# Performance work log

Hardware: AMD Instinct MI355X
Metric: run time of the kernel (lower is better)

## Reference

```python
import jax, jax.numpy as jnp
import numpy as np

WS = 8          # window_size
SHIFT = WS // 2 # shift for 'SW' type
HEADS = 6
HD = 32


def setup_inputs() -> dict:
    key = jax.random.key(0)
    ks = jax.random.split(key, 6)
    return {
        "x": jax.random.normal(ks[0], (4, 256, 256, 192), jnp.float32),
        "w_qkv": jax.random.normal(ks[1], (192, 576), jnp.float32) * 0.02,
        "b_qkv": jax.random.normal(ks[2], (576,), jnp.float32) * 0.02,
        "rel_pos": jax.random.normal(ks[3], (HEADS, 2 * WS - 1, 2 * WS - 1), jnp.float32) * 0.02,
        "w_out": jax.random.normal(ks[4], (192, 192), jnp.float32) * 0.02,
        "b_out": jax.random.normal(ks[5], (192,), jnp.float32) * 0.02,
    }


def reference(x, w_qkv, b_qkv, rel_pos, w_out, b_out):
    b, h, w, c = x.shape
    scale = HD ** (-0.5)
    wa = WS * WS  # window area
    # shifted-window roll
    x = jnp.roll(x, (-SHIFT, -SHIFT), axis=(1, 2))
    hw, ww = h // WS, w // WS
    nw = hw * ww
    # partition into windows: [b, nw, wa, c]
    xw = x.reshape(b, hw, WS, ww, WS, c).transpose(0, 1, 3, 2, 4, 5).reshape(b, nw, wa, c)
    qkv = xw @ w_qkv + b_qkv                       # [b, nw, wa, 3c]
    qkv = qkv.reshape(b, nw, wa, 3, HEADS, HD)
    q = qkv[..., 0, :, :] * scale
    k = qkv[..., 1, :, :]
    v = qkv[..., 2, :, :]
    attn = jnp.einsum('bnqhd,bnkhd->bnhqk', q, k)  # [b, nw, heads, wa, wa]
    # relative position bias
    coords = jnp.stack(jnp.meshgrid(jnp.arange(WS), jnp.arange(WS), indexing='ij')).reshape(2, -1).T  # [wa,2]
    rel = coords[:, None, :] - coords[None, :, :] + WS - 1   # [wa, wa, 2]
    bias = rel_pos[:, rel[..., 0], rel[..., 1]]              # [heads, wa, wa]
    attn = attn + bias[None, None]
    # shift mask (only last window masked, per the module's generate_mask)
    s = WS - SHIFT
    mask = jnp.zeros((nw, wa, wa), bool)
    mask = mask.at[-1, :s, s:].set(True).at[-1, s:, :s].set(True)
    attn = jnp.where(mask[None, :, None], -jnp.inf, attn)
    attn = jax.nn.softmax(attn, axis=-1)
    out = jnp.einsum('bnhqk,bnkhd->bnqhd', attn, v)          # [b, nw, wa, heads, hd]
    out = out.reshape(b, hw, ww, WS, WS, c).transpose(0, 1, 3, 2, 4, 5).reshape(b, h, w, c)
    out = out @ w_out + b_out
    out = jnp.roll(out, (SHIFT, SHIFT), axis=(1, 2))
    return out
```

## Files before the change

### kernel.cpp

```cpp
#include <hip/hip_runtime.h>
#include <hip/hip_bf16.h>

typedef __attribute__((ext_vector_type(8))) short short8;
typedef __attribute__((ext_vector_type(4))) float f32x4;

#define MFMA(a, b, c) __builtin_amdgcn_mfma_f32_16x16x32_bf16((a), (b), (c), 0, 0, 0)

namespace {
constexpr int IMG = 256;
constexpr int NWIN = 1024;
constexpr float SCALE = 0.17677669529663687f;
constexpr float L2E   = 1.4426950408889634f;
}

__device__ __forceinline__ unsigned pack2(float a, float b) {
    __hip_bfloat162 h = __float22bfloat162_rn(make_float2(a, b));
    union { __hip_bfloat162 h; unsigned u; } v; v.h = h;
    return v.u;
}

__global__ __launch_bounds__(256)
void prep_all(const float* __restrict__ w_qkv, const float* __restrict__ w_out,
              const float* __restrict__ rel_pos, const float* __restrict__ b_qkv,
              unsigned short* __restrict__ wqT, unsigned short* __restrict__ woT,
              float* __restrict__ biasf, float* __restrict__ bq2) {
    const int bx = blockIdx.x;
    const int t  = threadIdx.x;
    if (bx < 72) {
        __shared__ float tile[32][65];
        const float* in; unsigned short* out; int N, scale_n; float scale; int tx, ty;
        if (bx < 54) { in = w_qkv; out = wqT; N = 576; scale_n = 192; scale = SCALE; tx = bx % 9; ty = bx / 9; }
        else { const int b2 = bx - 54; in = w_out; out = woT; N = 192; scale_n = 0; scale = 1.0f; tx = b2 % 3; ty = b2 / 3; }
        const int nb = tx * 64, kb = ty * 32;
        const int tn = t & 63, tk = t >> 6;
#pragma unroll
        for (int p = 0; p < 8; ++p)
            tile[p * 4 + tk][tn] = in[(size_t)(kb + p * 4 + tk) * N + nb + tn];
        __syncthreads();
        const int n = t >> 2, kc = (t & 3) * 8;
        const float s = (nb + n) < scale_n ? scale : 1.0f;
        uint4 u;
        u.x = pack2(tile[kc + 0][n] * s, tile[kc + 1][n] * s);
        u.y = pack2(tile[kc + 2][n] * s, tile[kc + 3][n] * s);
        u.z = pack2(tile[kc + 4][n] * s, tile[kc + 5][n] * s);
        u.w = pack2(tile[kc + 6][n] * s, tile[kc + 7][n] * s);
        *(uint4*)(out + (size_t)(nb + n) * 192 + kb + kc) = u;
    } else {
        const int o = (bx - 72) * 256 + t;
        const int k = o & 63, q = (o >> 6) & 63, h = o >> 12;
        const int qy = q >> 3, qx = q & 7, ky = k >> 3, kx = k & 7;
        const float bv = rel_pos[h * 225 + (qy - ky + 7) * 15 + (qx - kx + 7)] * L2E;
        biasf[o] = bv;
        const bool masked = (q < 4) != (k < 4);
        biasf[24576 + o] = masked ? -30000.0f : bv;
        if (bx == 72) {
            for (int i = t; i < 576; i += 256)
                bq2[i] = b_qkv[i] * (i < 192 ? SCALE : 1.0f);
        }
    }
}

__global__ __launch_bounds__(256, 3)
void wmsa_fused(const float* __restrict__ x,
                const float* __restrict__ bq2,
                const float* __restrict__ biasf,
                const unsigned short* __restrict__ wqT,
                const unsigned short* __restrict__ woT,
                const float* __restrict__ b_out,
                float* __restrict__ out) {
    __shared__ unsigned short x_s[64][200];
    __shared__ unsigned short qp_s[64][72];
    __shared__ unsigned short kp_s[64][72];
    __shared__ unsigned short vT_s[64][72];

    const int tid = threadIdx.x;
    const int w   = tid >> 6;
    const int l   = tid & 63;
    const int l15 = l & 15, lg = l >> 4;
    const int wing = blockIdx.x;
    const int b   = wing >> 10;
    const int win = wing & (NWIN - 1);
    const int wy  = win >> 5, wx = win & 31;
    const float* bias_t = biasf + ((win == NWIN - 1) ? 24576 : 0);

    {
        const int t  = tid >> 2;
        const int c0 = tid & 3;
        const int pr = ((wy << 3) + (t >> 3) + 4) & (IMG - 1);
        const int pc = ((wx << 3) + (t & 7) + 4) & (IMG - 1);
        const float* xrow = x + ((size_t)((b * IMG + pr) * IMG + pc)) * 192;
#pragma unroll
        for (int i = 0; i < 12; ++i) {
            const int c = c0 + 4 * i;
            const float4 xv = *reinterpret_cast<const float4*>(xrow + c * 4);
            uint2 pk; pk.x = pack2(xv.x, xv.y); pk.y = pack2(xv.z, xv.w);
            *(uint2*)(&x_s[t][c * 4]) = pk;
        }
    }
    __syncthreads();

    const int h_loc = w >> 1;
    const int qt0   = 2 * (w & 1);

    f32x4 g2[3][4];
#pragma unroll
    for (int mi = 0; mi < 3; ++mi) {
        const float4 bo = *reinterpret_cast<const float4*>(b_out + 16 * (w + 4 * mi) + 4 * lg);
        const f32x4 c0 = {bo.x, bo.y, bo.z, bo.w};
#pragma unroll
        for (int nt = 0; nt < 4; ++nt) g2[mi][nt] = c0;
    }

#pragma unroll 1
    for (int g = 0; g < 3; ++g) {
        f32x4 aq[3][4];
        const unsigned short* wp[3];
#pragma unroll
        for (int ci = 0; ci < 3; ++ci) {
            const int t = w + 4 * ci;
            const int which = t >> 2, sub = t & 3;
            const int hh = sub >> 1, d0 = (sub & 1) * 16;
            const int grow = which * 192 + (2 * g + hh) * 32 + d0 + l15;
            wp[ci] = wqT + (size_t)grow * 192 + lg * 8;
            f32x4 c0;
            if (which < 2) {
                const float4 b4 = *reinterpret_cast<const float4*>(
                    bq2 + which * 192 + (2 * g + hh) * 32 + d0 + 4 * lg);
                c0 = f32x4{b4.x, b4.y, b4.z, b4.w};
            } else {
                const float bb = bq2[384 + (2 * g + hh) * 32 + d0 + l15];
                c0 = f32x4{bb, bb, bb, bb};
            }
#pragma unroll
            for (int nt = 0; nt < 4; ++nt) aq[ci][nt] = c0;
        }

        __builtin_amdgcn_s_setprio(1);
#pragma unroll
        for (int ks = 0; ks < 6; ++ks) {
            short8 xf[4];
#pragma unroll
            for (int nt = 0; nt < 4; ++nt)
                xf[nt] = *(const short8*)(&x_s[16 * nt + l15][ks * 32 + lg * 8]);
#pragma unroll
            for (int ci = 0; ci < 3; ++ci) {
                const short8 wf = *(const short8*)wp[ci];
                wp[ci] += 32;
                if (ci < 2 ? ((w + 4 * ci) >> 2) < 2 : ((w + 8) >> 2) < 2) {
#pragma unroll
                    for (int nt = 0; nt < 4; ++nt) aq[ci][nt] = MFMA(wf, xf[nt], aq[ci][nt]);
                } else {
#pragma unroll
                    for (int nt = 0; nt < 4; ++nt) aq[ci][nt] = MFMA(xf[nt], wf, aq[ci][nt]);
                }
            }
        }
        __builtin_amdgcn_s_setprio(0);

#pragma unroll
        for (int ci = 0; ci < 3; ++ci) {
            const int t = w + 4 * ci;
            const int which = t >> 2, sub = t & 3;
            const int hh = sub >> 1, d0 = (sub & 1) * 16;
            if (which < 2) {
                const int rbase = hh * 32 + d0 + 4 * lg;
#pragma unroll
                for (int nt = 0; nt < 4; ++nt) {
                    const int tok = 16 * nt + l15;
                    uint2 pk;
                    pk.x = pack2(aq[ci][nt][0], aq[ci][nt][1]);
                    pk.y = pack2(aq[ci][nt][2], aq[ci][nt][3]);
                    if (which == 0) *(uint2*)(&qp_s[tok][rbase]) = pk;
                    else            *(uint2*)(&kp_s[tok][rbase]) = pk;
                }
            } else {
                const int dcol = hh * 32 + d0 + l15;
#pragma unroll
                for (int nt = 0; nt < 4; ++nt) {
                    uint2 pk;
                    pk.x = pack2(aq[ci][nt][0], aq[ci][nt][1]);
                    pk.y = pack2(aq[ci][nt][2], aq[ci][nt][3]);
                    *(uint2*)(&vT_s[dcol][16 * nt + 4 * lg]) = pk;
                }
            }
        }
        __syncthreads();

        short8 qf[2], kf[4];
#pragma unroll
        for (int mq = 0; mq < 2; ++mq)
            qf[mq] = *(const short8*)(&qp_s[16 * (qt0 + mq) + l15][h_loc * 32 + lg * 8]);
#pragma unroll
        for (int nt = 0; nt < 4; ++nt)
            kf[nt] = *(const short8*)(&kp_s[16 * nt + l15][h_loc * 32 + lg * 8]);
        f32x4 s[2][4];
        const f32x4 z = {0.f, 0.f, 0.f, 0.f};
        __builtin_amdgcn_s_setprio(1);
#pragma unroll
        for (int mq = 0; mq < 2; ++mq)
#pragma unroll
            for (int nt = 0; nt < 4; ++nt) s[mq][nt] = MFMA(kf[nt], qf[mq], z);
        __builtin_amdgcn_s_setprio(0);
        __syncthreads();

        unsigned short (*p_buf)[72] = (h_loc == 0) ? qp_s : kp_s;
        const int h = 2 * g + h_loc;
        float ri[2];
#pragma unroll
        for (int mq = 0; mq < 2; ++mq) {
            const int q = 16 * (qt0 + mq) + l15;
            const float* bq = bias_t + ((h * 64 + q) << 6) + 4 * lg;
            float e[4][4], sum = 0.f;
#pragma unroll
            for (int nt = 0; nt < 4; ++nt) {
                const float4 bb = *(const float4*)(bq + 16 * nt);
                e[nt][0] = __builtin_exp2f(fmaf(s[mq][nt][0], L2E, bb.x));
                e[nt][1] = __builtin_exp2f(fmaf(s[mq][nt][1], L2E, bb.y));
                e[nt][2] = __builtin_exp2f(fmaf(s[mq][nt][2], L2E, bb.z));
                e[nt][3] = __builtin_exp2f(fmaf(s[mq][nt][3], L2E, bb.w));
                sum += (e[nt][0] + e[nt][1]) + (e[nt][2] + e[nt][3]);
            }
            sum += __shfl_xor(sum, 16);
            sum += __shfl_xor(sum, 32);
            ri[mq] = __builtin_amdgcn_rcpf(sum);
#pragma unroll
            for (int nt = 0; nt < 4; ++nt) {
                uint2 pk;
                pk.x = pack2(e[nt][0], e[nt][1]);
                pk.y = pack2(e[nt][2], e[nt][3]);
                *(uint2*)(&p_buf[q][16 * nt + 4 * lg]) = pk;
            }
        }

        f32x4 o[2][2];
#pragma unroll
        for (int dm = 0; dm < 2; ++dm)
#pragma unroll
            for (int qn = 0; qn < 2; ++qn) o[dm][qn] = z;
        __builtin_amdgcn_s_setprio(1);
#pragma unroll
        for (int ks2 = 0; ks2 < 2; ++ks2) {
            short8 pf[2];
#pragma unroll
            for (int qn = 0; qn < 2; ++qn)
                pf[qn] = *(const short8*)(&p_buf[16 * (qt0 + qn) + l15][ks2 * 32 + lg * 8]);
#pragma unroll
            for (int dm = 0; dm < 2; ++dm) {
                const short8 vf = *(const short8*)(&vT_s[h_loc * 32 + 16 * dm + l15][ks2 * 32 + lg * 8]);
#pragma unroll
                for (int qn = 0; qn < 2; ++qn) o[dm][qn] = MFMA(vf, pf[qn], o[dm][qn]);
            }
        }
        __builtin_amdgcn_s_setprio(0);
#pragma unroll
        for (int dm = 0; dm < 2; ++dm)
#pragma unroll
            for (int qn = 0; qn < 2; ++qn) {
                const int tok = 16 * (qt0 + qn) + l15;
                const float rr = ri[qn];
                uint2 pk;
                pk.x = pack2(o[dm][qn][0] * rr, o[dm][qn][1] * rr);
                pk.y = pack2(o[dm][qn][2] * rr, o[dm][qn][3] * rr);
                *(uint2*)(&p_buf[tok][16 * dm + 4 * lg]) = pk;
            }
        __syncthreads();

        __builtin_amdgcn_s_setprio(1);
#pragma unroll
        for (int ks2 = 0; ks2 < 2; ++ks2) {
            short8 bfr[4];
#pragma unroll
            for (int nt = 0; nt < 4; ++nt)
                bfr[nt] = (ks2 == 0)
                    ? *(const short8*)(&qp_s[16 * nt + l15][lg * 8])
                    : *(const short8*)(&kp_s[16 * nt + l15][lg * 8]);
#pragma unroll
            for (int mi = 0; mi < 3; ++mi) {
                const int oct = w + 4 * mi;
                const short8 af = *(const short8*)(
                    woT + (size_t)(16 * oct + l15) * 192 + g * 64 + ks2 * 32 + lg * 8);
#pragma unroll
                for (int nt = 0; nt < 4; ++nt) g2[mi][nt] = MFMA(af, bfr[nt], g2[mi][nt]);
            }
        }
        __builtin_amdgcn_s_setprio(0);
        if (g < 2) __syncthreads();
    }

#pragma unroll
    for (int nt = 0; nt < 4; ++nt) {
        const int tok = 16 * nt + l15;
        const int pr = ((wy << 3) + (tok >> 3) + 4) & (IMG - 1);
        const int pc = ((wx << 3) + (tok & 7) + 4) & (IMG - 1);
        float* orow = out + (size_t)((b * IMG + pr) * IMG + pc) * 192;
#pragma unroll
        for (int mi = 0; mi < 3; ++mi) {
            const int oc0 = 16 * (w + 4 * mi) + 4 * lg;
            *reinterpret_cast<float4*>(orow + oc0) =
                make_float4(g2[mi][nt][0], g2[mi][nt][1], g2[mi][nt][2], g2[mi][nt][3]);
        }
    }
}

extern "C" void kernel_launch(void* const* d_in, const int* in_sizes, int n_in,
                              void* d_out, int out_size, void* d_ws, size_t ws_size,
                              hipStream_t stream) {
    (void)in_sizes; (void)n_in; (void)out_size; (void)ws_size;
    const float* x       = (const float*)d_in[0];
    const float* w_qkv   = (const float*)d_in[1];
    const float* b_qkv   = (const float*)d_in[2];
    const float* rel_pos = (const float*)d_in[3];
    const float* w_out   = (const float*)d_in[4];
    const float* b_out   = (const float*)d_in[5];
    float* out = (float*)d_out;

    unsigned short* wqT   = (unsigned short*)d_ws;
    unsigned short* woT   = wqT + 576 * 192;
    float*          biasf = (float*)(woT + 192 * 192);
    float*          bq2   = biasf + 2 * 24576;

    prep_all<<<dim3(168), dim3(256), 0, stream>>>(
        w_qkv, w_out, rel_pos, b_qkv, wqT, woT, biasf, bq2);

    wmsa_fused<<<dim3(4 * NWIN), dim3(256), 0, stream>>>(
        x, bq2, biasf, wqT, woT, b_out, out);
}
```

Before: 277.6 us.

## Process one head per iteration to shrink LDS and registers for higher occupancy

The fused window-attention loop now handles one head per iteration over six iterations, where it previously handled two heads per iteration over three. The Q, K and V^T shared buffers shrink to one head's width and the QKV accumulators drop from three to two tiles per wave. The launch bound rises from 3 to 4 blocks per CU. The cost is twice as many loop iterations and __syncthreads barriers, and only two of the four waves compute V, so work per wave is uneven during the projection.

```diff
diff --git a/kernel.cpp b/kernel.cpp
--- a/kernel.cpp
+++ b/kernel.cpp
@@ -60,7 +60,7 @@
     }
 }
 
-__global__ __launch_bounds__(256, 3)
+__global__ __launch_bounds__(256, 4)
 void wmsa_fused(const float* __restrict__ x,
                 const float* __restrict__ bq2,
                 const float* __restrict__ biasf,
@@ -69,9 +69,9 @@
                 const float* __restrict__ b_out,
                 float* __restrict__ out) {
     __shared__ unsigned short x_s[64][200];
-    __shared__ unsigned short qp_s[64][72];
-    __shared__ unsigned short kp_s[64][72];
-    __shared__ unsigned short vT_s[64][72];
+    __shared__ unsigned short q_s[64][40];
+    __shared__ unsigned short k_s[64][40];
+    __shared__ unsigned short vT_s[32][72];
 
     const int tid = threadIdx.x;
     const int w   = tid >> 6;
@@ -99,8 +99,10 @@
     }
     __syncthreads();
 
-    const int h_loc = w >> 1;
-    const int qt0   = 2 * (w & 1);
+    const int whichA = w >> 1;
+    const int d0A    = (w & 1) * 16;
+    const bool hasB  = (w < 2);
+    const int d0B    = (w & 1) * 16;
 
     f32x4 g2[3][4];
 #pragma unroll
@@ -112,28 +114,21 @@
     }
 
 #pragma unroll 1
-    for (int g = 0; g < 3; ++g) {
-        f32x4 aq[3][4];
-        const unsigned short* wp[3];
-#pragma unroll
-        for (int ci = 0; ci < 3; ++ci) {
-            const int t = w + 4 * ci;
-            const int which = t >> 2, sub = t & 3;
-            const int hh = sub >> 1, d0 = (sub & 1) * 16;
-            const int grow = which * 192 + (2 * g + hh) * 32 + d0 + l15;
-            wp[ci] = wqT + (size_t)grow * 192 + lg * 8;
-            f32x4 c0;
-            if (which < 2) {
-                const float4 b4 = *reinterpret_cast<const float4*>(
-                    bq2 + which * 192 + (2 * g + hh) * 32 + d0 + 4 * lg);
-                c0 = f32x4{b4.x, b4.y, b4.z, b4.w};
-            } else {
-                const float bb = bq2[384 + (2 * g + hh) * 32 + d0 + l15];
-                c0 = f32x4{bb, bb, bb, bb};
-            }
-#pragma unroll
-            for (int nt = 0; nt < 4; ++nt) aq[ci][nt] = c0;
-        }
+    for (int h = 0; h < 6; ++h) {
+        f32x4 aqA[4], aqB[4];
+        {
+            const float4 b4 = *reinterpret_cast<const float4*>(
+                bq2 + whichA * 192 + h * 32 + d0A + 4 * lg);
+            const f32x4 cA = {b4.x, b4.y, b4.z, b4.w};
+            const float bb = bq2[384 + h * 32 + d0B + l15];
+            const f32x4 cB = {bb, bb, bb, bb};
+#pragma unroll
+            for (int nt = 0; nt < 4; ++nt) { aqA[nt] = cA; aqB[nt] = cB; }
+        }
+        const unsigned short* wpA =
+            wqT + (size_t)(whichA * 192 + h * 32 + d0A + l15) * 192 + lg * 8;
+        const unsigned short* wpB =
+            wqT + (size_t)(384 + h * 32 + d0B + l15) * 192 + lg * 8;
 
         __builtin_amdgcn_s_setprio(1);
 #pragma unroll
@@ -142,149 +137,120 @@
 #pragma unroll
             for (int nt = 0; nt < 4; ++nt)
                 xf[nt] = *(const short8*)(&x_s[16 * nt + l15][ks * 32 + lg * 8]);
-#pragma unroll
-            for (int ci = 0; ci < 3; ++ci) {
-                const short8 wf = *(const short8*)wp[ci];
-                wp[ci] += 32;
-                if (ci < 2 ? ((w + 4 * ci) >> 2) < 2 : ((w + 8) >> 2) < 2) {
-#pragma unroll
-                    for (int nt = 0; nt < 4; ++nt) aq[ci][nt] = MFMA(wf, xf[nt], aq[ci][nt]);
-                } else {
-#pragma unroll
-                    for (int nt = 0; nt < 4; ++nt) aq[ci][nt] = MFMA(xf[nt], wf, aq[ci][nt]);
-                }
+            const short8 wfA = *(const short8*)wpA;  wpA += 32;
+#pragma unroll
+            for (int nt = 0; nt < 4; ++nt) aqA[nt] = MFMA(wfA, xf[nt], aqA[nt]);
+            if (hasB) {
+                const short8 wfB = *(const short8*)wpB;  wpB += 32;
+#pragma unroll
+                for (int nt = 0; nt < 4; ++nt) aqB[nt] = MFMA(xf[nt], wfB, aqB[nt]);
             }
         }
         __builtin_amdgcn_s_setprio(0);
 
-#pragma unroll
-        for (int ci = 0; ci < 3; ++ci) {
-            const int t = w + 4 * ci;
-            const int which = t >> 2, sub = t & 3;
-            const int hh = sub >> 1, d0 = (sub & 1) * 16;
-            if (which < 2) {
-                const int rbase = hh * 32 + d0 + 4 * lg;
-#pragma unroll
-                for (int nt = 0; nt < 4; ++nt) {
-                    const int tok = 16 * nt + l15;
-                    uint2 pk;
-                    pk.x = pack2(aq[ci][nt][0], aq[ci][nt][1]);
-                    pk.y = pack2(aq[ci][nt][2], aq[ci][nt][3]);
-                    if (which == 0) *(uint2*)(&qp_s[tok][rbase]) = pk;
-                    else            *(uint2*)(&kp_s[tok][rbase]) = pk;
-                }
-            } else {
-                const int dcol = hh * 32 + d0 + l15;
+        {
+            unsigned short (*tgtA)[40] = (whichA == 0) ? q_s : k_s;
+#pragma unroll
+            for (int nt = 0; nt < 4; ++nt) {
+                const int tok = 16 * nt + l15;
+                uint2 pk;
+                pk.x = pack2(aqA[nt][0], aqA[nt][1]);
+                pk.y = pack2(aqA[nt][2], aqA[nt][3]);
+                *(uint2*)(&tgtA[tok][d0A + 4 * lg]) = pk;
+            }
+            if (hasB) {
 #pragma unroll
                 for (int nt = 0; nt < 4; ++nt) {
                     uint2 pk;
-                    pk.x = pack2(aq[ci][nt][0], aq[ci][nt][1]);
-                    pk.y = pack2(aq[ci][nt][2], aq[ci][nt][3]);
-                    *(uint2*)(&vT_s[dcol][16 * nt + 4 * lg]) = pk;
+                    pk.x = pack2(aqB[nt][0], aqB[nt][1]);
+                    pk.y = pack2(aqB[nt][2], aqB[nt][3]);
+                    *(uint2*)(&vT_s[d0B + l15][16 * nt + 4 * lg]) = pk;
                 }
             }
         }
         __syncthreads();
 
-        short8 qf[2], kf[4];
-#pragma unroll
-        for (int mq = 0; mq < 2; ++mq)
-            qf[mq] = *(const short8*)(&qp_s[16 * (qt0 + mq) + l15][h_loc * 32 + lg * 8]);
+        const short8 qf = *(const short8*)(&q_s[16 * w + l15][lg * 8]);
+        short8 kf[4];
 #pragma unroll
         for (int nt = 0; nt < 4; ++nt)
-            kf[nt] = *(const short8*)(&kp_s[16 * nt + l15][h_loc * 32 + lg * 8]);
-        f32x4 s[2][4];
+            kf[nt] = *(const short8*)(&k_s[16 * nt + l15][lg * 8]);
+        f32x4 s[4];
         const f32x4 z = {0.f, 0.f, 0.f, 0.f};
         __builtin_amdgcn_s_setprio(1);
 #pragma unroll
-        for (int mq = 0; mq < 2; ++mq)
-#pragma unroll
-            for (int nt = 0; nt < 4; ++nt) s[mq][nt] = MFMA(kf[nt], qf[mq], z);
+        for (int nt = 0; nt < 4; ++nt) s[nt] = MFMA(kf[nt], qf, z);
         __builtin_amdgcn_s_setprio(0);
         __syncthreads();
 
-        unsigned short (*p_buf)[72] = (h_loc == 0) ? qp_s : kp_s;
-        const int h = 2 * g + h_loc;
-        float ri[2];
-#pragma unroll
-        for (int mq = 0; mq < 2; ++mq) {
-            const int q = 16 * (qt0 + mq) + l15;
+        float ri;
+        {
+            const int q = 16 * w + l15;
             const float* bq = bias_t + ((h * 64 + q) << 6) + 4 * lg;
             float e[4][4], sum = 0.f;
 #pragma unroll
             for (int nt = 0; nt < 4; ++nt) {
                 const float4 bb = *(const float4*)(bq + 16 * nt);
-                e[nt][0] = __builtin_exp2f(fmaf(s[mq][nt][0], L2E, bb.x));
-                e[nt][1] = __builtin_exp2f(fmaf(s[mq][nt][1], L2E, bb.y));
-                e[nt][2] = __builtin_exp2f(fmaf(s[mq][nt][2], L2E, bb.z));
-                e[nt][3] = __builtin_exp2f(fmaf(s[mq][nt][3], L2E, bb.w));
+                e[nt][0] = __builtin_exp2f(fmaf(s[nt][0], L2E, bb.x));
+                e[nt][1] = __builtin_exp2f(fmaf(s[nt][1], L2E, bb.y));
+                e[nt][2] = __builtin_exp2f(fmaf(s[nt][2], L2E, bb.z));
+                e[nt][3] = __builtin_exp2f(fmaf(s[nt][3], L2E, bb.w));
                 sum += (e[nt][0] + e[nt][1]) + (e[nt][2] + e[nt][3]);
             }
             sum += __shfl_xor(sum, 16);
             sum += __shfl_xor(sum, 32);
-            ri[mq] = __builtin_amdgcn_rcpf(sum);
+            ri = __builtin_amdgcn_rcpf(sum);
 #pragma unroll
             for (int nt = 0; nt < 4; ++nt) {
                 uint2 pk;
                 pk.x = pack2(e[nt][0], e[nt][1]);
                 pk.y = pack2(e[nt][2], e[nt][3]);
-                *(uint2*)(&p_buf[q][16 * nt + 4 * lg]) = pk;
-            }
-        }
-
-        f32x4 o[2][2];
-#pragma unroll
-        for (int dm = 0; dm < 2; ++dm)
-#pragma unroll
-            for (int qn = 0; qn < 2; ++qn) o[dm][qn] = z;
+                if (nt < 2) *(uint2*)(&q_s[q][16 * nt + 4 * lg]) = pk;
+                else        *(uint2*)(&k_s[q][16 * (nt - 2) + 4 * lg]) = pk;
+            }
+        }
+
+        f32x4 o[2] = {z, z};
+        {
+            const short8 pf0 = *(const short8*)(&q_s[16 * w + l15][lg * 8]);
+            const short8 pf1 = *(const short8*)(&k_s[16 * w + l15][lg * 8]);
+            __builtin_amdgcn_s_setprio(1);
+#pragma unroll
+            for (int dm = 0; dm < 2; ++dm) {
+                const short8 vf0 = *(const short8*)(&vT_s[16 * dm + l15][lg * 8]);
+                const short8 vf1 = *(const short8*)(&vT_s[16 * dm + l15][32 + lg * 8]);
+                o[dm] = MFMA(vf0, pf0, o[dm]);
+                o[dm] = MFMA(vf1, pf1, o[dm]);
+            }
+            __builtin_amdgcn_s_setprio(0);
+        }
+#pragma unroll
+        for (int dm = 0; dm < 2; ++dm) {
+            const int tok = 16 * w + l15;
+            uint2 pk;
+            pk.x = pack2(o[dm][0] * ri, o[dm][1] * ri);
+            pk.y = pack2(o[dm][2] * ri, o[dm][3] * ri);
+            *(uint2*)(&q_s[tok][16 * dm + 4 * lg]) = pk;
+        }
+        __syncthreads();
+
         __builtin_amdgcn_s_setprio(1);
-#pragma unroll
-        for (int ks2 = 0; ks2 < 2; ++ks2) {
-            short8 pf[2];
-#pragma unroll
-            for (int qn = 0; qn < 2; ++qn)
-                pf[qn] = *(const short8*)(&p_buf[16 * (qt0 + qn) + l15][ks2 * 32 + lg * 8]);
-#pragma unroll
-            for (int dm = 0; dm < 2; ++dm) {
-                const short8 vf = *(const short8*)(&vT_s[h_loc * 32 + 16 * dm + l15][ks2 * 32 + lg * 8]);
-#pragma unroll
-                for (int qn = 0; qn < 2; ++qn) o[dm][qn] = MFMA(vf, pf[qn], o[dm][qn]);
-            }
-        }
-        __builtin_amdgcn_s_setprio(0);
-#pragma unroll
-        for (int dm = 0; dm < 2; ++dm)
-#pragma unroll
-            for (int qn = 0; qn < 2; ++qn) {
-                const int tok = 16 * (qt0 + qn) + l15;
-                const float rr = ri[qn];
-                uint2 pk;
-                pk.x = pack2(o[dm][qn][0] * rr, o[dm][qn][1] * rr);
-                pk.y = pack2(o[dm][qn][2] * rr, o[dm][qn][3] * rr);
-                *(uint2*)(&p_buf[tok][16 * dm + 4 * lg]) = pk;
-            }
-        __syncthreads();
-
-        __builtin_amdgcn_s_setprio(1);
-#pragma unroll
-        for (int ks2 = 0; ks2 < 2; ++ks2) {
+        {
             short8 bfr[4];
 #pragma unroll
             for (int nt = 0; nt < 4; ++nt)
-                bfr[nt] = (ks2 == 0)
-                    ? *(const short8*)(&qp_s[16 * nt + l15][lg * 8])
-                    : *(const short8*)(&kp_s[16 * nt + l15][lg * 8]);
+                bfr[nt] = *(const short8*)(&q_s[16 * nt + l15][lg * 8]);
 #pragma unroll
             for (int mi = 0; mi < 3; ++mi) {
                 const int oct = w + 4 * mi;
                 const short8 af = *(const short8*)(
-                    woT + (size_t)(16 * oct + l15) * 192 + g * 64 + ks2 * 32 + lg * 8);
+                    woT + (size_t)(16 * oct + l15) * 192 + h * 32 + lg * 8);
 #pragma unroll
                 for (int nt = 0; nt < 4; ++nt) g2[mi][nt] = MFMA(af, bfr[nt], g2[mi][nt]);
             }
         }
         __builtin_amdgcn_s_setprio(0);
-        if (g < 2) __syncthreads();
+        if (h < 5) __syncthreads();
     }
 
 #pragma unroll
```

Result: slower. 308.7 us (+11.2%).
